# Kernel tuning notes

Measured on AMD Instinct MI355X. Metric: run time of the kernel, lower is better.

## Reference

```python
import jax, jax.numpy as jnp
import numpy as np

BN_EPS = 1e-5
NEG_SLOPE = 0.2


def setup_inputs() -> dict:
    key = jax.random.key(0)
    k1, k2, k3 = jax.random.split(key, 3)
    B, C, N, K = 4, 64, 16384, 32
    x = jax.random.normal(k1, (B, C, N), dtype=jnp.float32)
    edges = jax.random.randint(k2, (B, N, K), 0, N, dtype=jnp.int64)
    W = jax.random.normal(k3, (C, C), dtype=jnp.float32) * 0.05  # [C_out, C_in]
    gamma = jnp.ones((C,), dtype=jnp.float32)
    beta = jnp.zeros((C,), dtype=jnp.float32)
    return {"x": x, "edges": edges, "W": W, "gamma": gamma, "beta": beta}


def reference(x, edges, W, gamma, beta):
    # x: [B, C, N], edges: [B, N, k] -> out: [B, C_out, N]
    pts = jnp.transpose(x, (0, 2, 1))            # [B, N, C]
    nb = jax.vmap(lambda p, e: p[e])(pts, edges)  # [B, N, k, C] batched gather
    agg = nb.mean(axis=2)                         # [B, N, C] neighbor mean
    h = jnp.einsum('bnc,oc->bon', agg, W)         # 1x1 conv, no bias -> [B, C_out, N]
    # BatchNorm1d (training-mode batch stats over batch and point dims)
    mu = h.mean(axis=(0, 2), keepdims=True)
    var = h.var(axis=(0, 2), keepdims=True)       # biased variance (as torch BN)
    hn = (h - mu) * jax.lax.rsqrt(var + BN_EPS)
    y = gamma[None, :, None] * hn + beta[None, :, None]
    return jnp.where(y > 0, y, NEG_SLOPE * y)     # LeakyReLU(0.2)
```

## Files before the change

kernel.cpp:

```cpp
#include <hip/hip_runtime.h>
#include <hip/hip_bf16.h>

#define BB 4
#define CC 64
#define NN 16384
#define KK 32
#define PTS (BB * NN)
#define NP  2048

static __device__ __forceinline__ unsigned short f2bf(float f) {
    unsigned u = __builtin_bit_cast(unsigned, f);
    unsigned r = (u + 0x7fffu + ((u >> 16) & 1u)) >> 16;
    return (unsigned short)r;
}
static __device__ __forceinline__ float bflo(unsigned u) {
    return __builtin_bit_cast(float, u << 16);
}
static __device__ __forceinline__ float bfhi(unsigned u) {
    return __builtin_bit_cast(float, u & 0xffff0000u);
}

template <int ZB>
__global__ __launch_bounds__(256) void k1_wx_t(const float* __restrict__ x,
                                               const float* __restrict__ W,
                                               unsigned* __restrict__ ztu,
                                               int b0) {
    __shared__ float    xs[64 * 65];
    __shared__ unsigned zsu[64 * 33];
    const int tid  = threadIdx.x;
    const int lane = tid & 63;
    const int w    = tid >> 6;
    const int chunk = blockIdx.x;
    const int bl = chunk >> 8;
    const int b  = b0 + bl;
    const int n0 = (chunk & 255) << 6;

    const float* xb = x + (size_t)b * CC * NN + n0;
#pragma unroll
    for (int i = 0; i < 16; ++i) {
        const int c = i * 4 + w;
        xs[c * 65 + lane] = xb[(size_t)c * NN + lane];
    }
    __syncthreads();

    float xr[64];
#pragma unroll
    for (int c = 0; c < 64; ++c) xr[c] = xs[c * 65 + lane];

    float acc[16];
#pragma unroll
    for (int i = 0; i < 16; ++i) {
        const int o = w * 16 + i;
        const unsigned long long wa = (unsigned long long)(const void*)(W + (o << 6));
        const unsigned plo = __builtin_amdgcn_readfirstlane((unsigned)wa);
        const unsigned phi = __builtin_amdgcn_readfirstlane((unsigned)(wa >> 32));
        const float* wrow = (const float*)(((unsigned long long)phi << 32) | plo);
        float a0 = 0.f, a1 = 0.f, a2 = 0.f, a3 = 0.f;
#pragma unroll
        for (int c = 0; c < 64; c += 4) {
            a0 = fmaf(wrow[c + 0], xr[c + 0], a0);
            a1 = fmaf(wrow[c + 1], xr[c + 1], a1);
            a2 = fmaf(wrow[c + 2], xr[c + 2], a2);
            a3 = fmaf(wrow[c + 3], xr[c + 3], a3);
        }
        acc[i] = (a0 + a1) + (a2 + a3);
    }

#pragma unroll
    for (int i = 0; i < 8; ++i)
        zsu[lane * 33 + w * 8 + i] =
            (unsigned)f2bf(acc[2 * i]) | ((unsigned)f2bf(acc[2 * i + 1]) << 16);
    __syncthreads();

    unsigned* zo = ztu + ((size_t)bl * NN + n0) * 32;
    const int r  = tid >> 2;
    const int c0 = (tid & 3) * 8;
    const unsigned* srow = &zsu[r * 33 + c0];
    uint4 v0, v1;
    v0.x = srow[0]; v0.y = srow[1]; v0.z = srow[2]; v0.w = srow[3];
    v1.x = srow[4]; v1.y = srow[5]; v1.z = srow[6]; v1.w = srow[7];
    *(uint4*)(zo + (size_t)r * 32 + c0)     = v0;
    *(uint4*)(zo + (size_t)r * 32 + c0 + 4) = v1;
}

template <int ZB>
__global__ __launch_bounds__(256) void k3_gather(const unsigned* __restrict__ ztu,
                                                 const int* __restrict__ edges,
                                                 float* __restrict__ hout,
                                                 float* __restrict__ p1,
                                                 float* __restrict__ p2,
                                                 int b0) {
    __shared__ float otile[64 * 33];
    __shared__ float red[4][64][4];
    const int tid  = threadIdx.x;
    const int lane = tid & 63;
    const int w    = tid >> 6;
    int bl, chunk;
    if (ZB == 4) {
        const int xcd = blockIdx.x & 7;
        bl    = xcd & 3;
        chunk = (((blockIdx.x >> 2) & 1) << 8) | (blockIdx.x >> 3);
    } else {
        bl = 0;
        chunk = blockIdx.x;
    }
    const int b  = b0 + bl;
    const int n0 = chunk << 5;
    const unsigned* zb = ztu + (size_t)bl * NN * 32 + (lane & 31);
    const int hi = lane >> 5;
    float s1a = 0.f, s2a = 0.f, s1b = 0.f, s2b = 0.f;

    const int pg0 = b * NN + n0 + w * 8;
    int myv[4];
#pragma unroll
    for (int i = 0; i < 4; ++i)
        myv[i] = edges[(size_t)(pg0 + 2 * i) * KK + lane];

#pragma unroll
    for (int i = 0; i < 4; ++i) {
        const int my = myv[i];
        float a0 = 0.f, a1 = 0.f;
#pragma unroll
        for (int kk = 0; kk < KK; kk += 8) {
            int e[8];
#pragma unroll
            for (int j = 0; j < 8; ++j) {
                const int e0 = __builtin_amdgcn_readlane(my, kk + j);
                const int e1 = __builtin_amdgcn_readlane(my, 32 + kk + j);
                e[j] = hi ? e1 : e0;
            }
            unsigned u[8];
#pragma unroll
            for (int j = 0; j < 8; ++j) u[j] = zb[(size_t)e[j] * 32];
#pragma unroll
            for (int j = 0; j < 8; ++j) { a0 += bflo(u[j]); a1 += bfhi(u[j]); }
        }
        const float h0 = a0 * (1.0f / KK);
        const float h1 = a1 * (1.0f / KK);
        s1a += h0; s2a += h0 * h0;
        s1b += h1; s2b += h1 * h1;
        const int pidx = w * 8 + 2 * i + hi;
        const int cp   = lane & 31;
        otile[(2 * cp)     * 33 + pidx] = h0;
        otile[(2 * cp + 1) * 33 + pidx] = h1;
    }
    __syncthreads();

    {
        const int row = tid >> 2;
        const int c0  = (tid & 3) * 8;
        const float* s = &otile[row * 33 + c0];
        float4 v0, v1;
        v0.x = s[0]; v0.y = s[1]; v0.z = s[2]; v0.w = s[3];
        v1.x = s[4]; v1.y = s[5]; v1.z = s[6]; v1.w = s[7];
        float* dst = hout + (size_t)b * CC * NN + (size_t)row * NN + n0 + c0;
        *(float4*)dst       = v0;
        *(float4*)(dst + 4) = v1;
    }

    red[w][lane][0] = s1a; red[w][lane][1] = s2a;
    red[w][lane][2] = s1b; red[w][lane][3] = s2b;
    __syncthreads();
    if (tid < 64) {
        const int cp = tid >> 1, sub = tid & 1;
        float t1 = 0.f, t2 = 0.f;
#pragma unroll
        for (int w2 = 0; w2 < 4; ++w2) {
            t1 += red[w2][cp][2 * sub]     + red[w2][cp + 32][2 * sub];
            t2 += red[w2][cp][2 * sub + 1] + red[w2][cp + 32][2 * sub + 1];
        }
        const int pslot = (ZB == 4) ? (bl * 512 + chunk) : (b0 * 512 + chunk);
        p1[pslot * 64 + tid] = t1;
        p2[pslot * 64 + tid] = t2;
    }
}

__global__ __launch_bounds__(1024) void k4_stats(const float* __restrict__ p1,
                                                 const float* __restrict__ p2,
                                                 const float* __restrict__ gamma,
                                                 const float* __restrict__ beta,
                                                 float* __restrict__ sc,
                                                 float* __restrict__ sh) {
    __shared__ float r1[1024], r2[1024];
    const int tid = threadIdx.x;
    float s1 = 0.f, s2 = 0.f;
    for (int i = tid; i < NP * 64; i += 1024) {
        s1 += p1[i];
        s2 += p2[i];
    }
    r1[tid] = s1;
    r2[tid] = s2;
    __syncthreads();
    if (tid < 64) {
        float t1 = 0.f, t2 = 0.f;
#pragma unroll
        for (int j = 0; j < 1024; j += 64) { t1 += r1[tid + j]; t2 += r2[tid + j]; }
        const float inv = 1.0f / (float)PTS;
        const float mu  = t1 * inv;
        const float var = t2 * inv - mu * mu;
        const float s   = gamma[tid] * rsqrtf(var + 1e-5f);
        sc[tid] = s;
        sh[tid] = beta[tid] - mu * s;
    }
}

__global__ __launch_bounds__(256) void k5_bn(float* __restrict__ out,
                                             const float* __restrict__ sc,
                                             const float* __restrict__ sh) {
    const int total4 = BB * CC * NN / 4;
    for (int i = blockIdx.x * 256 + threadIdx.x; i < total4; i += gridDim.x * 256) {
        const int c = (i >> 12) & 63;
        const float s = sc[c];
        const float t = sh[c];
        float4 v = ((const float4*)out)[i];
        float y;
        y = fmaf(v.x, s, t); v.x = y > 0.f ? y : 0.2f * y;
        y = fmaf(v.y, s, t); v.y = y > 0.f ? y : 0.2f * y;
        y = fmaf(v.z, s, t); v.z = y > 0.f ? y : 0.2f * y;
        y = fmaf(v.w, s, t); v.w = y > 0.f ? y : 0.2f * y;
        ((float4*)out)[i] = v;
    }
}

extern "C" void kernel_launch(void* const* d_in, const int* in_sizes, int n_in,
                              void* d_out, int out_size, void* d_ws, size_t ws_size,
                              hipStream_t stream) {
    const float* x     = (const float*)d_in[0];
    const int*   edges = (const int*)d_in[1];
    const float* W     = (const float*)d_in[2];
    const float* gamma = (const float*)d_in[3];
    const float* beta  = (const float*)d_in[4];
    float* out = (float*)d_out;

    const size_t ZT_FULL_U = (size_t)BB * NN * 32;
    const size_t ZT_ONE_U  = (size_t)NN * 32;
    const size_t PARTS_F   = (size_t)NP * 64 * 2 + 128;
    const bool full = ws_size >= (ZT_FULL_U + PARTS_F) * 4;

    unsigned* ztu = (unsigned*)d_ws;
    float* p1 = (float*)d_ws + (full ? ZT_FULL_U : ZT_ONE_U);
    float* p2 = p1 + (size_t)NP * 64;
    float* sc = p2 + (size_t)NP * 64;
    float* sh = sc + 64;

    if (full) {
        hipLaunchKernelGGL((k1_wx_t<BB>),   dim3(BB * 256), dim3(256), 0, stream,
                           x, W, ztu, 0);
        hipLaunchKernelGGL((k3_gather<BB>), dim3(2048), dim3(256), 0, stream,
                           ztu, edges, out, p1, p2, 0);
    } else {
        for (int b = 0; b < BB; ++b) {
            hipLaunchKernelGGL((k1_wx_t<1>),   dim3(256), dim3(256), 0, stream,
                               x, W, ztu, b);
            hipLaunchKernelGGL((k3_gather<1>), dim3(512), dim3(256), 0, stream,
                               ztu, edges, out, p1, p2, b);
        }
    }
    hipLaunchKernelGGL(k4_stats, dim3(1), dim3(1024), 0, stream, p1, p2, gamma, beta, sc, sh);
    hipLaunchKernelGGL(k5_bn, dim3(2048), dim3(256), 0, stream, out, sc, sh);
}
```

Measured before the change: 173.4 us.

## Gather neighbor rows with 8-byte loads split across lane groups

Restructures the gather kernel so each wavefront processes one point at a time, with 16 lanes each loading 8 bytes (4 bf16 channels) and 4 lane groups covering different neighbors. Partial sums are combined with cross-lane shuffles, and the per-block stats reduction is reorganized to match. This widens the per-lane loads and cuts the number of load instructions per neighbor row. In exchange it adds shuffle reductions, redundant per-lane stats accumulation, and edge loads issued per point.

```diff
diff --git a/kernel.cpp b/kernel.cpp
--- a/kernel.cpp
+++ b/kernel.cpp
@@ -91,10 +91,13 @@
                                                  float* __restrict__ p2,
                                                  int b0) {
     __shared__ float otile[64 * 33];
-    __shared__ float red[4][64][4];
+    __shared__ float red1[4][64][4];
+    __shared__ float red2[4][64][4];
     const int tid  = threadIdx.x;
     const int lane = tid & 63;
     const int w    = tid >> 6;
+    const int cp4  = lane & 15;
+    const int g    = lane >> 4;
     int bl, chunk;
     if (ZB == 4) {
         const int xcd = blockIdx.x & 7;
@@ -106,43 +109,44 @@
     }
     const int b  = b0 + bl;
     const int n0 = chunk << 5;
-    const unsigned* zb = ztu + (size_t)bl * NN * 32 + (lane & 31);
-    const int hi = lane >> 5;
-    float s1a = 0.f, s2a = 0.f, s1b = 0.f, s2b = 0.f;
-
-    const int pg0 = b * NN + n0 + w * 8;
-    int myv[4];
-#pragma unroll
-    for (int i = 0; i < 4; ++i)
-        myv[i] = edges[(size_t)(pg0 + 2 * i) * KK + lane];
-
-#pragma unroll
-    for (int i = 0; i < 4; ++i) {
-        const int my = myv[i];
-        float a0 = 0.f, a1 = 0.f;
-#pragma unroll
-        for (int kk = 0; kk < KK; kk += 8) {
-            int e[8];
-#pragma unroll
-            for (int j = 0; j < 8; ++j) {
-                const int e0 = __builtin_amdgcn_readlane(my, kk + j);
-                const int e1 = __builtin_amdgcn_readlane(my, 32 + kk + j);
-                e[j] = hi ? e1 : e0;
-            }
-            unsigned u[8];
-#pragma unroll
-            for (int j = 0; j < 8; ++j) u[j] = zb[(size_t)e[j] * 32];
-#pragma unroll
-            for (int j = 0; j < 8; ++j) { a0 += bflo(u[j]); a1 += bfhi(u[j]); }
-        }
-        const float h0 = a0 * (1.0f / KK);
-        const float h1 = a1 * (1.0f / KK);
-        s1a += h0; s2a += h0 * h0;
-        s1b += h1; s2b += h1 * h1;
-        const int pidx = w * 8 + 2 * i + hi;
-        const int cp   = lane & 31;
-        otile[(2 * cp)     * 33 + pidx] = h0;
-        otile[(2 * cp + 1) * 33 + pidx] = h1;
+    const uint2* zb2 = (const uint2*)(ztu + (size_t)bl * NN * 32);
+    float s1q0 = 0.f, s1q1 = 0.f, s1q2 = 0.f, s1q3 = 0.f;
+    float s2q0 = 0.f, s2q1 = 0.f, s2q2 = 0.f, s2q3 = 0.f;
+
+    for (int i = 0; i < 8; ++i) {
+        const int pl = w * 8 + i;
+        const int pg = b * NN + n0 + pl;
+        const int ebase = __builtin_amdgcn_readfirstlane(pg * KK);
+
+        int e[8];
+#pragma unroll
+        for (int kk = 0; kk < 8; ++kk)
+            e[kk] = edges[ebase + kk * 4 + g];
+
+        uint2 u[8];
+#pragma unroll
+        for (int kk = 0; kk < 8; ++kk)
+            u[kk] = zb2[((unsigned)e[kk] << 4) | (unsigned)cp4];
+
+        float a0 = 0.f, a1 = 0.f, a2 = 0.f, a3 = 0.f;
+#pragma unroll
+        for (int kk = 0; kk < 8; ++kk) {
+            a0 += bflo(u[kk].x); a1 += bfhi(u[kk].x);
+            a2 += bflo(u[kk].y); a3 += bfhi(u[kk].y);
+        }
+        a0 += __shfl_xor(a0, 16); a1 += __shfl_xor(a1, 16);
+        a2 += __shfl_xor(a2, 16); a3 += __shfl_xor(a3, 16);
+        a0 += __shfl_xor(a0, 32); a1 += __shfl_xor(a1, 32);
+        a2 += __shfl_xor(a2, 32); a3 += __shfl_xor(a3, 32);
+
+        const float h0 = a0 * (1.0f / KK), h1 = a1 * (1.0f / KK);
+        const float h2 = a2 * (1.0f / KK), h3 = a3 * (1.0f / KK);
+        s1q0 += h0; s2q0 += h0 * h0;
+        s1q1 += h1; s2q1 += h1 * h1;
+        s1q2 += h2; s2q2 += h2 * h2;
+        s1q3 += h3; s2q3 += h3 * h3;
+        const float hv = (g == 0) ? h0 : (g == 1) ? h1 : (g == 2) ? h2 : h3;
+        otile[(cp4 * 4 + g) * 33 + pl] = hv;
     }
     __syncthreads();
 
@@ -158,16 +162,18 @@
         *(float4*)(dst + 4) = v1;
     }
 
-    red[w][lane][0] = s1a; red[w][lane][1] = s2a;
-    red[w][lane][2] = s1b; red[w][lane][3] = s2b;
+    red1[w][lane][0] = s1q0; red1[w][lane][1] = s1q1;
+    red1[w][lane][2] = s1q2; red1[w][lane][3] = s1q3;
+    red2[w][lane][0] = s2q0; red2[w][lane][1] = s2q1;
+    red2[w][lane][2] = s2q2; red2[w][lane][3] = s2q3;
     __syncthreads();
     if (tid < 64) {
-        const int cp = tid >> 1, sub = tid & 1;
+        const int q = tid >> 2, j = tid & 3;
         float t1 = 0.f, t2 = 0.f;
 #pragma unroll
         for (int w2 = 0; w2 < 4; ++w2) {
-            t1 += red[w2][cp][2 * sub]     + red[w2][cp + 32][2 * sub];
-            t2 += red[w2][cp][2 * sub + 1] + red[w2][cp + 32][2 * sub + 1];
+            t1 += red1[w2][q][j];
+            t2 += red2[w2][q][j];
         }
         const int pslot = (ZB == 4) ? (bl * 512 + chunk) : (b0 * 512 + chunk);
         p1[pslot * 64 + tid] = t1;
```

Result: no change. 175.3 us (+1.1%).
